# Optimization experiments

Hardware: AMD Instinct MI355X
Metric: run time of the kernel (lower is better)

Reference implementation:

```python
import jax, jax.numpy as jnp
import numpy as np
import math

B, S, D, H, FF = 2, 2048, 1024, 16, 4096
HD = D // H
EPS = 1e-5


def setup_inputs() -> dict:
    key = jax.random.key(0)
    ks = jax.random.split(key, 16)
    w = lambda k, shape: (jax.random.normal(k, shape, jnp.float32) * 0.02)
    future = jnp.triu(jnp.ones((S, S), dtype=bool), k=1)
    causal_mask = jnp.where(future, -jnp.inf, 0.0).astype(jnp.float32)
    return {
        "src": jax.random.normal(ks[0], (B, S, D), jnp.float32),
        "causal_mask": causal_mask,
        "Wq": w(ks[1], (D, D)), "bq": jnp.zeros((D,), jnp.float32),
        "Wk": w(ks[2], (D, D)), "bk": jnp.zeros((D,), jnp.float32),
        "Wv": w(ks[3], (D, D)), "bv": jnp.zeros((D,), jnp.float32),
        "Wo": w(ks[4], (D, D)), "bo": jnp.zeros((D,), jnp.float32),
        "W1": w(ks[5], (D, FF)), "b1": jnp.zeros((FF,), jnp.float32),
        "W2": w(ks[6], (FF, D)), "b2": jnp.zeros((D,), jnp.float32),
        "ln1_g": jnp.ones((D,), jnp.float32), "ln1_b": jnp.zeros((D,), jnp.float32),
        "ln2_g": jnp.ones((D,), jnp.float32), "ln2_b": jnp.zeros((D,), jnp.float32),
    }


def _layernorm(x, g, b):
    mu = jnp.mean(x, axis=-1, keepdims=True)
    var = jnp.mean((x - mu) ** 2, axis=-1, keepdims=True)
    return (x - mu) * jax.lax.rsqrt(var + EPS) * g + b


def reference(src, causal_mask, Wq, bq, Wk, bk, Wv, bv, Wo, bo,
              W1, b1, W2, b2, ln1_g, ln1_b, ln2_g, ln2_b):
    # QKV projections, split heads: [B,S,D] -> [B,H,S,HD]
    def split_heads(x):
        return x.reshape(B, S, H, HD).transpose(0, 2, 1, 3)

    q = split_heads(src @ Wq + bq)
    k = split_heads(src @ Wk + bk)
    v = split_heads(src @ Wv + bv)

    # scores: [B,H,S,S]; attn_mask = causal_mask broadcast over batch, then head dim
    scores = jnp.einsum("bhqd,bhkd->bhqk", q, k) / math.sqrt(HD)
    scores = scores + causal_mask[None, None, :, :]
    # scores[scores != scores] = 0
    scores = jnp.where(jnp.isnan(scores), 0.0, scores)
    # rows that are entirely inf -> 0
    mask_all_inf = jnp.all(jnp.isinf(scores), axis=-1, keepdims=True)
    scores = jnp.where(mask_all_inf, 0.0, scores)
    attn = jax.nn.softmax(scores, axis=-1)
    attn = jnp.where(jnp.isnan(attn), 0.0, attn)

    ctx = jnp.einsum("bhqk,bhkd->bhqd", attn, v)
    ctx = ctx.transpose(0, 2, 1, 3).reshape(B, S, D)
    attn_out = ctx @ Wo + bo

    x = _layernorm(src + attn_out, ln1_g, ln1_b)
    ff = jax.nn.relu(x @ W1 + b1) @ W2 + b2
    return _layernorm(x + ff, ln2_g, ln2_b)
```

## Files before the change

kernel.cpp:

```cpp
#include <hip/hip_runtime.h>

#define SS 2048
#define DD 1024
#define HH 16
#define HDIM 64
#define BB 2
#define FFD 4096
#define MR (BB*SS)
#define QKVLD 3072

typedef __bf16 bf16;
typedef __bf16 bf16x4 __attribute__((ext_vector_type(4)));
typedef __bf16 bf16x8 __attribute__((ext_vector_type(8)));
typedef float f32x4 __attribute__((ext_vector_type(4)));

struct P4 { bf16* p[4]; };

__device__ inline f32x4 mfma32(bf16x8 a, bf16x8 b, f32x4 c) {
  return __builtin_amdgcn_mfma_f32_16x16x32_bf16(a, b, c, 0, 0, 0);
}

__device__ inline void gload_lds16(const void* g, void* l) {
  __builtin_amdgcn_global_load_lds(
      (const __attribute__((address_space(1))) void*)g,
      (__attribute__((address_space(3))) void*)l, 16, 0, 0);
}

__global__ __launch_bounds__(256)
void cvt_bf16_kernel(const float* __restrict__ in, bf16* __restrict__ out, int n) {
  int i = (blockIdx.x * 256 + threadIdx.x) * 4;
  if (i >= n) return;
  float4 v = *(const float4*)(in + i);
  bf16x4 o;
  o[0] = (bf16)v.x; o[1] = (bf16)v.y; o[2] = (bf16)v.z; o[3] = (bf16)v.w;
  *(bf16x4*)(out + i) = o;
}

__global__ __launch_bounds__(256)
void concat_bias_kernel(const float* __restrict__ bq, const float* __restrict__ bk,
                        const float* __restrict__ bv, float* __restrict__ out) {
  int i = blockIdx.x * 256 + threadIdx.x;
  out[i] = i < 1024 ? bq[i] : (i < 2048 ? bk[i - 1024] : bv[i - 2048]);
}

__global__ __launch_bounds__(256)
void transpose_w_kernel(const float* __restrict__ W, bf16* __restrict__ Wt,
                        int K, int N) {
  __shared__ float t[32][33];
  int tx = threadIdx.x & 31, ty = threadIdx.x >> 5;
  int n0 = blockIdx.x * 32, k0 = blockIdx.y * 32;
  #pragma unroll
  for (int i = 0; i < 4; ++i)
    t[ty + i*8][tx] = W[(size_t)(k0 + ty + i*8) * N + n0 + tx];
  __syncthreads();
  #pragma unroll
  for (int i = 0; i < 4; ++i)
    Wt[(size_t)(n0 + ty + i*8) * K + k0 + tx] = (bf16)t[tx][ty + i*8];
}

__global__ __launch_bounds__(256)
void transpose_v_kernel(const bf16* __restrict__ V2d, bf16* __restrict__ Vt) {
  __shared__ bf16 t[32][33];
  int tx = threadIdx.x & 31, ty = threadIdx.x >> 5;
  int s0 = blockIdx.x * 32, d0 = blockIdx.y * 32;
  int bh = blockIdx.z;
  int b = bh >> 4, h = bh & 15;
  #pragma unroll
  for (int i = 0; i < 4; ++i)
    t[ty + i*8][tx] = V2d[(size_t)(b*SS + s0 + ty + i*8) * QKVLD + h*HDIM + d0 + tx];
  __syncthreads();
  #pragma unroll
  for (int i = 0; i < 4; ++i)
    Vt[((size_t)bh*HDIM + d0 + ty + i*8) * SS + s0 + tx] = t[tx][ty + i*8];
}

template<int OUT_BF16, int RELU, int SPLITK>
__global__ __launch_bounds__(512)
void gemm256(const bf16* __restrict__ A, const bf16* __restrict__ Bt,
             const float* __restrict__ bias, void* __restrict__ Cout,
             P4 part, int Ndim, int Kdim) {
  __shared__ bf16 Asm[2][256 * 64];
  __shared__ bf16 Bsm[2][256 * 64];
  const int gx = gridDim.x, gy = gridDim.y;
  const int gxy = gx * gy;
  const int nwg = gxy * gridDim.z;
  const int lin = (blockIdx.z * gy + blockIdx.y) * gx + blockIdx.x;
  const int swz = (lin & 7) * (nwg >> 3) + (lin >> 3);
  int bz = 0, rem = swz;
  if (SPLITK > 1) { bz = swz / gxy; rem = swz - bz * gxy; }
  const int by = rem / gx, bx = rem - by * gx;
  const int m0 = by * 256, n0 = bx * 256;
  const int tid = threadIdx.x;
  const int wave = tid >> 6, lane = tid & 63;
  const int g = lane >> 4, r = lane & 15;
  const int wr = wave >> 2, wn = wave & 3;
  const int kstart = bz * (Kdim / SPLITK);

  const int srow = wave * 8 + (lane >> 3);
  const int skslot = (lane & 7) ^ (lane >> 3);
  const bf16* Ag = A + (size_t)(m0 + srow) * Kdim + kstart + skslot * 8;
  const bf16* Bg = Bt + (size_t)(n0 + srow) * Kdim + kstart + skslot * 8;

  f32x4 acc[8][4] = {};
  const int NT = (Kdim / SPLITK) >> 6;

  auto stage = [&](int t) {
    const int kb = t << 6;
    bf16* Ad = Asm[t & 1];
    bf16* Bd = Bsm[t & 1];
    #pragma unroll
    for (int j = 0; j < 4; ++j)
      gload_lds16(Ag + (size_t)j * 64 * Kdim + kb, Ad + (j * 64 + wave * 8) * 64);
    #pragma unroll
    for (int j = 0; j < 4; ++j)
      gload_lds16(Bg + (size_t)j * 64 * Kdim + kb, Bd + (j * 64 + wave * 8) * 64);
  };

  stage(0);
  asm volatile("s_waitcnt vmcnt(0)" ::: "memory");
  asm volatile("s_barrier" ::: "memory");

  for (int t = 0; t < NT; ++t) {
    const bf16* Ab = Asm[t & 1];
    const bf16* Bb = Bsm[t & 1];
    #pragma unroll
    for (int ph = 0; ph < 4; ++ph) {
      const int mq = ph >> 1, nq = ph & 1;
      bf16x8 af[4][2], bfr[2][2];
      #pragma unroll
      for (int i = 0; i < 4; ++i) {
        const int row = wr * 128 + (mq * 4 + i) * 16 + r;
        #pragma unroll
        for (int kk = 0; kk < 2; ++kk)
          af[i][kk] = *(const bf16x8*)(Ab + row * 64 + (((kk * 4 + g) ^ (r & 7)) * 8));
      }
      #pragma unroll
      for (int i = 0; i < 2; ++i) {
        const int rowb = wn * 64 + (nq * 2 + i) * 16 + r;
        #pragma unroll
        for (int kk = 0; kk < 2; ++kk)
          bfr[i][kk] = *(const bf16x8*)(Bb + rowb * 64 + (((kk * 4 + g) ^ (r & 7)) * 8));
      }
      if (ph == 0 && t + 1 < NT) stage(t + 1);
      asm volatile("s_barrier" ::: "memory");
      __builtin_amdgcn_s_setprio(1);
      #pragma unroll
      for (int i = 0; i < 4; ++i)
        #pragma unroll
        for (int jn = 0; jn < 2; ++jn)
          #pragma unroll
          for (int kk = 0; kk < 2; ++kk)
            acc[mq * 4 + i][nq * 2 + jn] =
                mfma32(af[i][kk], bfr[jn][kk], acc[mq * 4 + i][nq * 2 + jn]);
      __builtin_amdgcn_s_setprio(0);
      asm volatile("s_barrier" ::: "memory");
    }
    asm volatile("s_waitcnt vmcnt(0)" ::: "memory");
    asm volatile("s_barrier" ::: "memory");
  }

  #pragma unroll
  for (int mi = 0; mi < 8; ++mi) {
    #pragma unroll
    for (int ni = 0; ni < 4; ++ni) {
      const int col = n0 + wn * 64 + ni * 16 + r;
      const float bv = (SPLITK > 1) ? 0.f : bias[col];
      #pragma unroll
      for (int jj = 0; jj < 4; ++jj) {
        const int row = m0 + wr * 128 + mi * 16 + g * 4 + jj;
        float v = acc[mi][ni][jj] + bv;
        if (RELU) v = fmaxf(v, 0.f);
        if (SPLITK > 1) part.p[bz][(size_t)row * Ndim + col] = (bf16)v;
        else if (OUT_BF16) ((bf16*)Cout)[(size_t)row * Ndim + col] = (bf16)v;
        else               ((float*)Cout)[(size_t)row * Ndim + col] = v;
      }
    }
  }
}

template<int OUT_BF16, int RELU, int SPLITK>
__global__ __launch_bounds__(256)
void gemm_bt(const bf16* __restrict__ A, const bf16* __restrict__ Bt,
             const float* __restrict__ bias, void* __restrict__ Cout,
             float* __restrict__ Cout2, int Mdim, int Ndim, int Kdim) {
  __shared__ bf16 As[128 * 32];
  __shared__ bf16 Bs[128 * 32];
  const int gx = gridDim.x, gy = gridDim.y;
  const int nwg = gx * gy * gridDim.z;
  const int lin = (blockIdx.z * gy + blockIdx.y) * gx + blockIdx.x;
  const int swz = (lin & 7) * (nwg >> 3) + (lin >> 3);
  const int bz = swz / (gx * gy);
  const int rem = swz - bz * gx * gy;
  const int by = rem / gx;
  const int bx = rem - by * gx;
  const int tid = threadIdx.x;
  const int wave = tid >> 6;
  const int lane = tid & 63;
  const int g = lane >> 4;
  const int r = lane & 15;
  const int m0 = by * 128;
  const int n0 = bx * 128;
  const int kchunk = Kdim / SPLITK;
  const int kstart = bz * kchunk;
  const int wr = wave >> 1, wc = wave & 1;
  f32x4 acc[4][4] = {};
  const int strow = tid >> 2;
  const int stcol = (tid & 3) * 8;
  const bf16* Abase = A + (size_t)(m0 + strow) * Kdim + kstart + stcol;
  const bf16* Bbase = Bt + (size_t)(n0 + strow) * Kdim + kstart + stcol;
  bf16* AsW = As + wave * 512;
  bf16* BsW = Bs + wave * 512;
  for (int k0 = 0; k0 < kchunk; k0 += 32) {
    __syncthreads();
    gload_lds16(Abase + k0, AsW);
    gload_lds16(Abase + k0 + (size_t)64 * Kdim, AsW + 2048);
    gload_lds16(Bbase + k0, BsW);
    gload_lds16(Bbase + k0 + (size_t)64 * Kdim, BsW + 2048);
    __syncthreads();
    bf16x8 af[4], bfr[4];
    #pragma unroll
    for (int i = 0; i < 4; ++i)
      af[i] = *(const bf16x8*)(As + (wr*64 + i*16 + r) * 32 + g * 8);
    #pragma unroll
    for (int i = 0; i < 4; ++i)
      bfr[i] = *(const bf16x8*)(Bs + (wc*64 + i*16 + r) * 32 + g * 8);
    #pragma unroll
    for (int mi = 0; mi < 4; ++mi)
      #pragma unroll
      for (int ni = 0; ni < 4; ++ni)
        acc[mi][ni] = mfma32(af[mi], bfr[ni], acc[mi][ni]);
  }
  float* outp = (SPLITK > 1 && bz) ? Cout2 : (float*)Cout;
  #pragma unroll
  for (int mi = 0; mi < 4; ++mi) {
    #pragma unroll
    for (int ni = 0; ni < 4; ++ni) {
      const int col = n0 + wc*64 + ni*16 + r;
      const float bv = (SPLITK > 1) ? 0.f : bias[col];
      #pragma unroll
      for (int j = 0; j < 4; ++j) {
        const int row = m0 + wr*64 + mi*16 + g*4 + j;
        float v = acc[mi][ni][j] + bv;
        if (RELU) v = fmaxf(v, 0.f);
        if (OUT_BF16) ((bf16*)Cout)[(size_t)row * Ndim + col] = (bf16)v;
        else          outp[(size_t)row * Ndim + col] = v;
      }
    }
  }
}

__global__ __launch_bounds__(256)
void attn_kernel(const bf16* __restrict__ Q2d, const bf16* __restrict__ K2d,
                 const bf16* __restrict__ Vt, bf16* __restrict__ ctx) {
  __shared__ bf16 Ks[2 * 4096];
  __shared__ bf16 Vs[2 * 4096];
  const int tid = threadIdx.x;
  const int wave = tid >> 6;
  const int lane = tid & 63;
  const int g = lane >> 4, r = lane & 15;
  const int lin = blockIdx.y * gridDim.x + blockIdx.x;
  const int swz = (lin & 7) * 64 + (lin >> 3);
  const int p = swz & 15;
  const int bh = swz >> 4;
  const int b = bh >> 4, h = bh & 15;

  const int strow = wave * 16 + (lane >> 2);
  const int lslot = (lane & 3) ^ ((lane >> 3) & 3);
  const bf16* srcK0 = K2d + (size_t)(b*SS + strow) * QKVLD + h*HDIM + lslot * 8;
  const bf16* srcK1 = srcK0 + 32;
  const bf16* srcV0 = Vt + ((size_t)bh*HDIM + strow) * SS + lslot * 8;
  const bf16* srcV1 = srcV0 + 32;

  auto sw = [](int row, int s) { return row * 32 + ((s ^ ((row >> 1) & 3)) * 8); };

  const int kr0 = 8 * (r >> 2) + (r & 3);
  const int oKa0 = sw(kr0,      g), oKb0 = 2048 + oKa0;
  const int oKa1 = sw(kr0 +  4, g), oKb1 = 2048 + oKa1;
  const int oKa2 = sw(kr0 + 32, g), oKb2 = 2048 + oKa2;
  const int oKa3 = sw(kr0 + 36, g), oKb3 = 2048 + oKa3;
  int oV[4];
  #pragma unroll
  for (int c = 0; c < 4; ++c) oV[c] = sw(c * 16 + r, g);

  #pragma unroll
  for (int tt = 0; tt < 2; ++tt) {
    const int tile = tt ? (31 - p) : p;
    const int q0 = tile * 64 + wave * 16;
    const int qg = q0 + r;
    const bf16* qp = Q2d + (size_t)(b*SS + q0 + r) * QKVLD + h * HDIM;
    const bf16x8 qf0 = *(const bf16x8*)(qp + g * 8);
    const bf16x8 qf1 = *(const bf16x8*)(qp + 32 + g * 8);
    f32x4 ov[4] = {};
    float m = -3.0e38f, l = 0.f;
    const int nst = tile + 1;
    {
      bf16* kb = Ks + wave * 512;
      bf16* vb = Vs + wave * 512;
      gload_lds16(srcK0, kb);
      gload_lds16(srcK1, kb + 2048);
      gload_lds16(srcV0, vb);
      gload_lds16(srcV1, vb + 2048);
    }
    __syncthreads();
    int cur = 0;
    for (int st = 0; st < nst; ++st) {
      const int k0 = st * 64;
      if (st + 1 < nst) {
        const int kn = k0 + 64;
        bf16* kb = Ks + (cur ^ 1) * 4096 + wave * 512;
        bf16* vb = Vs + (cur ^ 1) * 4096 + wave * 512;
        gload_lds16(srcK0 + (size_t)kn * QKVLD, kb);
        gload_lds16(srcK1 + (size_t)kn * QKVLD, kb + 2048);
        gload_lds16(srcV0 + kn, vb);
        gload_lds16(srcV1 + kn, vb + 2048);
      }
      const bf16* Kb = Ks + cur * 4096;
      const bf16* Vb = Vs + cur * 4096;
      f32x4 c0 = {}, c1 = {}, c2 = {}, c3 = {};
      __builtin_amdgcn_s_setprio(1);
      c0 = mfma32(*(const bf16x8*)(Kb + oKa0), qf0, c0);
      c1 = mfma32(*(const bf16x8*)(Kb + oKa1), qf0, c1);
      c2 = mfma32(*(const bf16x8*)(Kb + oKa2), qf0, c2);
      c3 = mfma32(*(const bf16x8*)(Kb + oKa3), qf0, c3);
      c0 = mfma32(*(const bf16x8*)(Kb + oKb0), qf1, c0);
      c1 = mfma32(*(const bf16x8*)(Kb + oKb1), qf1, c1);
      c2 = mfma32(*(const bf16x8*)(Kb + oKb2), qf1, c2);
      c3 = mfma32(*(const bf16x8*)(Kb + oKb3), qf1, c3);
      __builtin_amdgcn_s_setprio(0);
      float p0[4], p1[4], p2[4], p3[4];
      float tmax = -3.0e38f;
      const bool need_mask = (k0 + 63 > qg);
      #pragma unroll
      for (int j = 0; j < 4; ++j) {
        float s0 = c0[j] * 0.125f;
        float s1 = c1[j] * 0.125f;
        float s2 = c2[j] * 0.125f;
        float s3 = c3[j] * 0.125f;
        if (need_mask) {
          if (k0 + 8*g + j > qg)          s0 = -3.0e38f;
          if (k0 + 8*g + 4 + j > qg)      s1 = -3.0e38f;
          if (k0 + 32 + 8*g + j > qg)     s2 = -3.0e38f;
          if (k0 + 32 + 8*g + 4 + j > qg) s3 = -3.0e38f;
        }
        p0[j] = s0; p1[j] = s1; p2[j] = s2; p3[j] = s3;
        tmax = fmaxf(tmax, fmaxf(fmaxf(s0, s1), fmaxf(s2, s3)));
      }
      tmax = fmaxf(tmax, __shfl_xor(tmax, 16));
      tmax = fmaxf(tmax, __shfl_xor(tmax, 32));
      const float mnew = fmaxf(m, tmax);
      const float sc = __expf(m - mnew);
      float tsum = 0.f;
      #pragma unroll
      for (int j = 0; j < 4; ++j) {
        p0[j] = __expf(p0[j] - mnew);
        p1[j] = __expf(p1[j] - mnew);
        p2[j] = __expf(p2[j] - mnew);
        p3[j] = __expf(p3[j] - mnew);
        tsum += (p0[j] + p1[j]) + (p2[j] + p3[j]);
      }
      tsum += __shfl_xor(tsum, 16);
      tsum += __shfl_xor(tsum, 32);
      l = l * sc + tsum;
      m = mnew;
      bf16x8 pfa, pfb;
      #pragma unroll
      for (int j = 0; j < 4; ++j) {
        pfa[j] = (bf16)p0[j]; pfa[4 + j] = (bf16)p1[j];
        pfb[j] = (bf16)p2[j]; pfb[4 + j] = (bf16)p3[j];
      }
      #pragma unroll
      for (int j = 0; j < 4; ++j) {
        const float scj = __shfl(sc, 4*g + j);
        #pragma unroll
        for (int c = 0; c < 4; ++c) ov[c][j] *= scj;
      }
      __builtin_amdgcn_s_setprio(1);
      #pragma unroll
      for (int c = 0; c < 4; ++c) {
        bf16x8 vfa = *(const bf16x8*)(Vb + oV[c]);
        bf16x8 vfb = *(const bf16x8*)(Vb + 2048 + oV[c]);
        ov[c] = mfma32(pfa, vfa, ov[c]);
        ov[c] = mfma32(pfb, vfb, ov[c]);
      }
      __builtin_amdgcn_s_setprio(0);
      __syncthreads();
      cur ^= 1;
    }
    #pragma unroll
    for (int j = 0; j < 4; ++j) {
      const float lj = __shfl(l, 4*g + j);
      const float inv = 1.f / lj;
      const int row = b*SS + q0 + 4*g + j;
      #pragma unroll
      for (int c = 0; c < 4; ++c)
        ctx[(size_t)row * DD + h*HDIM + c*16 + r] = (bf16)(ov[c][j] * inv);
    }
  }
}

template<int NP, int HASB, int WRITEB>
__global__ __launch_bounds__(256)
void ln_kernel(const float* __restrict__ a, const float* __restrict__ p0,
               const float* __restrict__ p1, const float* __restrict__ cb,
               const float* __restrict__ gam, const float* __restrict__ bet,
               float* __restrict__ outf, bf16* __restrict__ outb) {
  const int row = blockIdx.x;
  const int tid = threadIdx.x;
  const size_t base = (size_t)row * DD + tid * 4;
  float4 va = *(const float4*)(a + base);
  float4 vc = *(const float4*)(p0 + base);
  float x0 = va.x + vc.x, x1 = va.y + vc.y, x2 = va.z + vc.z, x3 = va.w + vc.w;
  if (NP > 1) {
    float4 vp = *(const float4*)(p1 + base);
    x0 += vp.x; x1 += vp.y; x2 += vp.z; x3 += vp.w;
  }
  if (HASB) {
    float4 vb4 = *(const float4*)(cb + tid * 4);
    x0 += vb4.x; x1 += vb4.y; x2 += vb4.z; x3 += vb4.w;
  }
  float s  = x0 + x1 + x2 + x3;
  float s2 = x0*x0 + x1*x1 + x2*x2 + x3*x3;
  #pragma unroll
  for (int off = 32; off > 0; off >>= 1) {
    s  += __shfl_xor(s,  off);
    s2 += __shfl_xor(s2, off);
  }
  __shared__ float red[8];
  const int wv = tid >> 6;
  if ((tid & 63) == 0) { red[wv] = s; red[wv + 4] = s2; }
  __syncthreads();
  s  = red[0] + red[1] + red[2] + red[3];
  s2 = red[4] + red[5] + red[6] + red[7];
  const float mu  = s * (1.f / DD);
  const float var = s2 * (1.f / DD) - mu * mu;
  const float rs  = rsqrtf(var + 1e-5f);
  float4 vg = *(const float4*)(gam + tid * 4);
  float4 vb = *(const float4*)(bet + tid * 4);
  float y0 = (x0 - mu) * rs * vg.x + vb.x;
  float y1 = (x1 - mu) * rs * vg.y + vb.y;
  float y2 = (x2 - mu) * rs * vg.z + vb.z;
  float y3 = (x3 - mu) * rs * vg.w + vb.w;
  float4 yo; yo.x = y0; yo.y = y1; yo.z = y2; yo.w = y3;
  *(float4*)(outf + base) = yo;
  if (WRITEB) {
    bf16x4 ob;
    ob[0] = (bf16)y0; ob[1] = (bf16)y1; ob[2] = (bf16)y2; ob[3] = (bf16)y3;
    *(bf16x4*)(outb + base) = ob;
  }
}

__global__ __launch_bounds__(256)
void ln_bf4_kernel(const float* __restrict__ a, P4 part, const float* __restrict__ cb,
                   const float* __restrict__ gam, const float* __restrict__ bet,
                   float* __restrict__ outf) {
  const int row = blockIdx.x;
  const int tid = threadIdx.x;
  const size_t base = (size_t)row * DD + tid * 4;
  float4 va = *(const float4*)(a + base);
  bf16x4 u0 = *(const bf16x4*)(part.p[0] + base);
  bf16x4 u1 = *(const bf16x4*)(part.p[1] + base);
  bf16x4 u2 = *(const bf16x4*)(part.p[2] + base);
  bf16x4 u3 = *(const bf16x4*)(part.p[3] + base);
  float4 vb4 = *(const float4*)(cb + tid * 4);
  float x0 = va.x + ((float)u0[0] + (float)u1[0]) + ((float)u2[0] + (float)u3[0]) + vb4.x;
  float x1 = va.y + ((float)u0[1] + (float)u1[1]) + ((float)u2[1] + (float)u3[1]) + vb4.y;
  float x2 = va.z + ((float)u0[2] + (float)u1[2]) + ((float)u2[2] + (float)u3[2]) + vb4.z;
  float x3 = va.w + ((float)u0[3] + (float)u1[3]) + ((float)u2[3] + (float)u3[3]) + vb4.w;
  float s  = x0 + x1 + x2 + x3;
  float s2 = x0*x0 + x1*x1 + x2*x2 + x3*x3;
  #pragma unroll
  for (int off = 32; off > 0; off >>= 1) {
    s  += __shfl_xor(s,  off);
    s2 += __shfl_xor(s2, off);
  }
  __shared__ float red[8];
  const int wv = tid >> 6;
  if ((tid & 63) == 0) { red[wv] = s; red[wv + 4] = s2; }
  __syncthreads();
  s  = red[0] + red[1] + red[2] + red[3];
  s2 = red[4] + red[5] + red[6] + red[7];
  const float mu  = s * (1.f / DD);
  const float var = s2 * (1.f / DD) - mu * mu;
  const float rs  = rsqrtf(var + 1e-5f);
  float4 vg = *(const float4*)(gam + tid * 4);
  float4 vb = *(const float4*)(bet + tid * 4);
  float4 yo;
  yo.x = (x0 - mu) * rs * vg.x + vb.x;
  yo.y = (x1 - mu) * rs * vg.y + vb.y;
  yo.z = (x2 - mu) * rs * vg.z + vb.z;
  yo.w = (x3 - mu) * rs * vg.w + vb.w;
  *(float4*)(outf + base) = yo;
}

extern "C" void kernel_launch(void* const* d_in, const int* in_sizes, int n_in,
                              void* d_out, int out_size, void* d_ws, size_t ws_size,
                              hipStream_t stream) {
  const float* src  = (const float*)d_in[0];
  const float* Wq   = (const float*)d_in[2];
  const float* bq   = (const float*)d_in[3];
  const float* Wk   = (const float*)d_in[4];
  const float* bk   = (const float*)d_in[5];
  const float* Wv   = (const float*)d_in[6];
  const float* bv   = (const float*)d_in[7];
  const float* Wo   = (const float*)d_in[8];
  const float* bo   = (const float*)d_in[9];
  const float* W1   = (const float*)d_in[10];
  const float* b1   = (const float*)d_in[11];
  const float* W2   = (const float*)d_in[12];
  const float* b2   = (const float*)d_in[13];
  const float* ln1g = (const float*)d_in[14];
  const float* ln1b = (const float*)d_in[15];
  const float* ln2g = (const float*)d_in[16];
  const float* ln2b = (const float*)d_in[17];

  char* ws = (char*)d_ws;
  const size_t MB = 1024 * 1024;
  bf16* wqkvt = (bf16*)(ws + 0 * MB);
  bf16* wot   = (bf16*)(ws + 6 * MB);
  bf16* w1t   = (bf16*)(ws + 8 * MB);
  bf16* w2t   = (bf16*)(ws + 16 * MB);
  bf16* bsrc  = (bf16*)(ws + 24 * MB);
  bf16* xb    = bsrc;
  bf16* qkv   = (bf16*)(ws + 32 * MB);
  bf16* vt    = (bf16*)(ws + 56 * MB);
  bf16* ctx   = (bf16*)(ws + 64 * MB);
  bf16* ff1   = qkv;
  float* xf   = (float*)(ws + 72 * MB);
  float* bqkv = (float*)(ws + 88 * MB);
  float* wo_p1 = (float*)(ws + 32 * MB);
  float* attn_out = (float*)d_out;
  float* outp  = (float*)d_out;
  P4 fp;
  fp.p[0] = (bf16*)(ws + 0 * MB);
  fp.p[1] = (bf16*)(ws + 8 * MB);
  fp.p[2] = (bf16*)(ws + 24 * MB);
  fp.p[3] = (bf16*)(ws + 64 * MB);

  cvt_bf16_kernel<<<(MR * DD) / 1024, 256, 0, stream>>>(src, bsrc, MR * DD);
  transpose_w_kernel<<<dim3(32, 32), 256, 0, stream>>>(Wq, wqkvt,             DD, DD);
  transpose_w_kernel<<<dim3(32, 32), 256, 0, stream>>>(Wk, wqkvt + 1024*1024, DD, DD);
  transpose_w_kernel<<<dim3(32, 32), 256, 0, stream>>>(Wv, wqkvt + 2048*1024, DD, DD);
  transpose_w_kernel<<<dim3(32, 32), 256, 0, stream>>>(Wo, wot, DD, DD);
  transpose_w_kernel<<<dim3(128, 32), 256, 0, stream>>>(W1, w1t, DD, FFD);
  transpose_w_kernel<<<dim3(32, 128), 256, 0, stream>>>(W2, w2t, FFD, DD);
  concat_bias_kernel<<<12, 256, 0, stream>>>(bq, bk, bv, bqkv);

  gemm256<1, 0, 1><<<dim3(QKVLD / 256, MR / 256), 512, 0, stream>>>(bsrc, wqkvt, bqkv, qkv, P4{}, QKVLD, DD);
  transpose_v_kernel<<<dim3(SS / 32, HDIM / 32, BB * HH), 256, 0, stream>>>(qkv + 2048, vt);

  attn_kernel<<<dim3(16, BB * HH), 256, 0, stream>>>(qkv, qkv + 1024, vt, ctx);

  gemm_bt<0, 0, 2><<<dim3(8, 32, 2), 256, 0, stream>>>(ctx, wot, nullptr, attn_out, wo_p1, MR, DD, DD);
  ln_kernel<2, 1, 1><<<MR, 256, 0, stream>>>(src, attn_out, wo_p1, bo, ln1g, ln1b, xf, xb);

  gemm256<1, 1, 1><<<dim3(FFD / 256, MR / 256), 512, 0, stream>>>(xb, w1t, b1, ff1, P4{}, FFD, DD);
  gemm256<0, 0, 4><<<dim3(DD / 256, MR / 256, 4), 512, 0, stream>>>(ff1, w2t, nullptr, nullptr, fp, DD, FFD);
  ln_bf4_kernel<<<MR, 256, 0, stream>>>(xf, fp, b2, ln2g, ln2b, outp);
}
```

Baseline: 255.0 us.

## Split attention into one block per query tile with lazy exp2 softmax rescale

The attention kernel previously had each block process a paired light and heavy causal tile. Now each block handles a single 64-row query tile, so the grid doubles, and the heaviest tiles are scheduled first. The softmax works in the exp2 domain with the scale folded into one FMA, and it rescales the running max and accumulators only when a wave-level threshold is exceeded. The LDS swizzle also gains an extra XOR term to reduce bank conflicts. The trade-offs are more blocks, each reloading Q and K/V setup, and a bounded-overflow approach that depends on the threshold choice.

```diff
diff --git a/kernel.cpp b/kernel.cpp
--- a/kernel.cpp
+++ b/kernel.cpp
@@ -259,19 +259,21 @@
   const int lane = tid & 63;
   const int g = lane >> 4, r = lane & 15;
   const int lin = blockIdx.y * gridDim.x + blockIdx.x;
-  const int swz = (lin & 7) * 64 + (lin >> 3);
-  const int p = swz & 15;
-  const int bh = swz >> 4;
+  const int swz = (lin & 7) * 128 + (lin >> 3);
+  const int bh = swz >> 5;
+  const int tile = 31 - (swz & 31);
   const int b = bh >> 4, h = bh & 15;
 
   const int strow = wave * 16 + (lane >> 2);
-  const int lslot = (lane & 3) ^ ((lane >> 3) & 3);
+  const int lslot = (lane & 3) ^ ((lane >> 3) & 3) ^ ((2 * wave + (lane >> 5)) & 3);
   const bf16* srcK0 = K2d + (size_t)(b*SS + strow) * QKVLD + h*HDIM + lslot * 8;
   const bf16* srcK1 = srcK0 + 32;
   const bf16* srcV0 = Vt + ((size_t)bh*HDIM + strow) * SS + lslot * 8;
   const bf16* srcV1 = srcV0 + 32;
 
-  auto sw = [](int row, int s) { return row * 32 + ((s ^ ((row >> 1) & 3)) * 8); };
+  auto sw = [](int row, int s) {
+    return row * 32 + ((s ^ ((row >> 1) & 3) ^ ((row >> 3) & 3)) * 8);
+  };
 
   const int kr0 = 8 * (r >> 2) + (r & 3);
   const int oKa0 = sw(kr0,      g), oKb0 = 2048 + oKa0;
@@ -282,119 +284,124 @@
   #pragma unroll
   for (int c = 0; c < 4; ++c) oV[c] = sw(c * 16 + r, g);
 
-  #pragma unroll
-  for (int tt = 0; tt < 2; ++tt) {
-    const int tile = tt ? (31 - p) : p;
-    const int q0 = tile * 64 + wave * 16;
-    const int qg = q0 + r;
-    const bf16* qp = Q2d + (size_t)(b*SS + q0 + r) * QKVLD + h * HDIM;
-    const bf16x8 qf0 = *(const bf16x8*)(qp + g * 8);
-    const bf16x8 qf1 = *(const bf16x8*)(qp + 32 + g * 8);
-    f32x4 ov[4] = {};
-    float m = -3.0e38f, l = 0.f;
-    const int nst = tile + 1;
-    {
-      bf16* kb = Ks + wave * 512;
-      bf16* vb = Vs + wave * 512;
-      gload_lds16(srcK0, kb);
-      gload_lds16(srcK1, kb + 2048);
-      gload_lds16(srcV0, vb);
-      gload_lds16(srcV1, vb + 2048);
-    }
-    __syncthreads();
-    int cur = 0;
-    for (int st = 0; st < nst; ++st) {
-      const int k0 = st * 64;
-      if (st + 1 < nst) {
-        const int kn = k0 + 64;
-        bf16* kb = Ks + (cur ^ 1) * 4096 + wave * 512;
-        bf16* vb = Vs + (cur ^ 1) * 4096 + wave * 512;
-        gload_lds16(srcK0 + (size_t)kn * QKVLD, kb);
-        gload_lds16(srcK1 + (size_t)kn * QKVLD, kb + 2048);
-        gload_lds16(srcV0 + kn, vb);
-        gload_lds16(srcV1 + kn, vb + 2048);
+  const int q0 = tile * 64 + wave * 16;
+  const int qg = q0 + r;
+  const bf16* qp = Q2d + (size_t)(b*SS + q0 + r) * QKVLD + h * HDIM;
+  const bf16x8 qf0 = *(const bf16x8*)(qp + g * 8);
+  const bf16x8 qf1 = *(const bf16x8*)(qp + 32 + g * 8);
+  f32x4 ov[4] = {};
+  const float K2 = 0.18033688f;
+  float m2 = 0.f, l = 0.f;
+  const int nst = tile + 1;
+  {
+    bf16* kb = Ks + wave * 512;
+    bf16* vb = Vs + wave * 512;
+    gload_lds16(srcK0, kb);
+    gload_lds16(srcK1, kb + 2048);
+    gload_lds16(srcV0, vb);
+    gload_lds16(srcV1, vb + 2048);
+  }
+  __syncthreads();
+  int cur = 0;
+  for (int st = 0; st < nst; ++st) {
+    const int k0 = st * 64;
+    if (st + 1 < nst) {
+      const int kn = k0 + 64;
+      bf16* kb = Ks + (cur ^ 1) * 4096 + wave * 512;
+      bf16* vb = Vs + (cur ^ 1) * 4096 + wave * 512;
+      gload_lds16(srcK0 + (size_t)kn * QKVLD, kb);
+      gload_lds16(srcK1 + (size_t)kn * QKVLD, kb + 2048);
+      gload_lds16(srcV0 + kn, vb);
+      gload_lds16(srcV1 + kn, vb + 2048);
+    }
+    const bf16* Kb = Ks + cur * 4096;
+    const bf16* Vb = Vs + cur * 4096;
+    f32x4 c0 = {}, c1 = {}, c2 = {}, c3 = {};
+    __builtin_amdgcn_s_setprio(1);
+    c0 = mfma32(*(const bf16x8*)(Kb + oKa0), qf0, c0);
+    c1 = mfma32(*(const bf16x8*)(Kb + oKa1), qf0, c1);
+    c2 = mfma32(*(const bf16x8*)(Kb + oKa2), qf0, c2);
+    c3 = mfma32(*(const bf16x8*)(Kb + oKa3), qf0, c3);
+    c0 = mfma32(*(const bf16x8*)(Kb + oKb0), qf1, c0);
+    c1 = mfma32(*(const bf16x8*)(Kb + oKb1), qf1, c1);
+    c2 = mfma32(*(const bf16x8*)(Kb + oKb2), qf1, c2);
+    c3 = mfma32(*(const bf16x8*)(Kb + oKb3), qf1, c3);
+    __builtin_amdgcn_s_setprio(0);
+    float f0[4], f1[4], f2[4], f3[4];
+    float tmax = -3.0e38f;
+    #pragma unroll
+    for (int j = 0; j < 4; ++j) {
+      f0[j] = fmaf(c0[j], K2, -m2);
+      f1[j] = fmaf(c1[j], K2, -m2);
+      f2[j] = fmaf(c2[j], K2, -m2);
+      f3[j] = fmaf(c3[j], K2, -m2);
+    }
+    if (k0 + 63 > q0) {
+      #pragma unroll
+      for (int j = 0; j < 4; ++j) {
+        if (k0 + 8*g + j > qg)          f0[j] = -3.0e38f;
+        if (k0 + 8*g + 4 + j > qg)      f1[j] = -3.0e38f;
+        if (k0 + 32 + 8*g + j > qg)     f2[j] = -3.0e38f;
+        if (k0 + 32 + 8*g + 4 + j > qg) f3[j] = -3.0e38f;
       }
-      const bf16* Kb = Ks + cur * 4096;
-      const bf16* Vb = Vs + cur * 4096;
-      f32x4 c0 = {}, c1 = {}, c2 = {}, c3 = {};
-      __builtin_amdgcn_s_setprio(1);
-      c0 = mfma32(*(const bf16x8*)(Kb + oKa0), qf0, c0);
-      c1 = mfma32(*(const bf16x8*)(Kb + oKa1), qf0, c1);
-      c2 = mfma32(*(const bf16x8*)(Kb + oKa2), qf0, c2);
-      c3 = mfma32(*(const bf16x8*)(Kb + oKa3), qf0, c3);
-      c0 = mfma32(*(const bf16x8*)(Kb + oKb0), qf1, c0);
-      c1 = mfma32(*(const bf16x8*)(Kb + oKb1), qf1, c1);
-      c2 = mfma32(*(const bf16x8*)(Kb + oKb2), qf1, c2);
-      c3 = mfma32(*(const bf16x8*)(Kb + oKb3), qf1, c3);
-      __builtin_amdgcn_s_setprio(0);
-      float p0[4], p1[4], p2[4], p3[4];
-      float tmax = -3.0e38f;
-      const bool need_mask = (k0 + 63 > qg);
+    }
+    #pragma unroll
+    for (int j = 0; j < 4; ++j)
+      tmax = fmaxf(tmax, fmaxf(fmaxf(f0[j], f1[j]), fmaxf(f2[j], f3[j])));
+    tmax = fmaxf(tmax, __shfl_xor(tmax, 16));
+    tmax = fmaxf(tmax, __shfl_xor(tmax, 32));
+    if (__any(tmax > 11.54f)) {
+      const float rmp = fmaxf(tmax, 0.f);
+      m2 += rmp;
+      const float sc = exp2f(-rmp);
+      l *= sc;
       #pragma unroll
       for (int j = 0; j < 4; ++j) {
-        float s0 = c0[j] * 0.125f;
-        float s1 = c1[j] * 0.125f;
-        float s2 = c2[j] * 0.125f;
-        float s3 = c3[j] * 0.125f;
-        if (need_mask) {
-          if (k0 + 8*g + j > qg)          s0 = -3.0e38f;
-          if (k0 + 8*g + 4 + j > qg)      s1 = -3.0e38f;
-          if (k0 + 32 + 8*g + j > qg)     s2 = -3.0e38f;
-          if (k0 + 32 + 8*g + 4 + j > qg) s3 = -3.0e38f;
-        }
-        p0[j] = s0; p1[j] = s1; p2[j] = s2; p3[j] = s3;
-        tmax = fmaxf(tmax, fmaxf(fmaxf(s0, s1), fmaxf(s2, s3)));
-      }
-      tmax = fmaxf(tmax, __shfl_xor(tmax, 16));
-      tmax = fmaxf(tmax, __shfl_xor(tmax, 32));
-      const float mnew = fmaxf(m, tmax);
-      const float sc = __expf(m - mnew);
-      float tsum = 0.f;
-      #pragma unroll
-      for (int j = 0; j < 4; ++j) {
-        p0[j] = __expf(p0[j] - mnew);
-        p1[j] = __expf(p1[j] - mnew);
-        p2[j] = __expf(p2[j] - mnew);
-        p3[j] = __expf(p3[j] - mnew);
-        tsum += (p0[j] + p1[j]) + (p2[j] + p3[j]);
-      }
-      tsum += __shfl_xor(tsum, 16);
-      tsum += __shfl_xor(tsum, 32);
-      l = l * sc + tsum;
-      m = mnew;
-      bf16x8 pfa, pfb;
-      #pragma unroll
-      for (int j = 0; j < 4; ++j) {
-        pfa[j] = (bf16)p0[j]; pfa[4 + j] = (bf16)p1[j];
-        pfb[j] = (bf16)p2[j]; pfb[4 + j] = (bf16)p3[j];
-      }
-      #pragma unroll
-      for (int j = 0; j < 4; ++j) {
+        f0[j] -= rmp; f1[j] -= rmp; f2[j] -= rmp; f3[j] -= rmp;
         const float scj = __shfl(sc, 4*g + j);
         #pragma unroll
         for (int c = 0; c < 4; ++c) ov[c][j] *= scj;
       }
-      __builtin_amdgcn_s_setprio(1);
-      #pragma unroll
-      for (int c = 0; c < 4; ++c) {
-        bf16x8 vfa = *(const bf16x8*)(Vb + oV[c]);
-        bf16x8 vfb = *(const bf16x8*)(Vb + 2048 + oV[c]);
-        ov[c] = mfma32(pfa, vfa, ov[c]);
-        ov[c] = mfma32(pfb, vfb, ov[c]);
-      }
-      __builtin_amdgcn_s_setprio(0);
-      __syncthreads();
-      cur ^= 1;
-    }
+    }
+    float tsum = 0.f;
+    float p0[4], p1[4], p2[4], p3[4];
     #pragma unroll
     for (int j = 0; j < 4; ++j) {
-      const float lj = __shfl(l, 4*g + j);
-      const float inv = 1.f / lj;
-      const int row = b*SS + q0 + 4*g + j;
-      #pragma unroll
-      for (int c = 0; c < 4; ++c)
-        ctx[(size_t)row * DD + h*HDIM + c*16 + r] = (bf16)(ov[c][j] * inv);
-    }
+      p0[j] = exp2f(f0[j]);
+      p1[j] = exp2f(f1[j]);
+      p2[j] = exp2f(f2[j]);
+      p3[j] = exp2f(f3[j]);
+      tsum += (p0[j] + p1[j]) + (p2[j] + p3[j]);
+    }
+    tsum += __shfl_xor(tsum, 16);
+    tsum += __shfl_xor(tsum, 32);
+    l += tsum;
+    bf16x8 pfa, pfb;
+    #pragma unroll
+    for (int j = 0; j < 4; ++j) {
+      pfa[j] = (bf16)p0[j]; pfa[4 + j] = (bf16)p1[j];
+      pfb[j] = (bf16)p2[j]; pfb[4 + j] = (bf16)p3[j];
+    }
+    __builtin_amdgcn_s_setprio(1);
+    #pragma unroll
+    for (int c = 0; c < 4; ++c) {
+      bf16x8 vfa = *(const bf16x8*)(Vb + oV[c]);
+      bf16x8 vfb = *(const bf16x8*)(Vb + 2048 + oV[c]);
+      ov[c] = mfma32(pfa, vfa, ov[c]);
+      ov[c] = mfma32(pfb, vfb, ov[c]);
+    }
+    __builtin_amdgcn_s_setprio(0);
+    __syncthreads();
+    cur ^= 1;
+  }
+  #pragma unroll
+  for (int j = 0; j < 4; ++j) {
+    const float lj = __shfl(l, 4*g + j);
+    const float inv = 1.f / lj;
+    const int row = b*SS + q0 + 4*g + j;
+    #pragma unroll
+    for (int c = 0; c < 4; ++c)
+      ctx[(size_t)row * DD + h*HDIM + c*16 + r] = (bf16)(ov[c][j] * inv);
   }
 }
 
@@ -548,7 +555,7 @@
   gemm256<1, 0, 1><<<dim3(QKVLD / 256, MR / 256), 512, 0, stream>>>(bsrc, wqkvt, bqkv, qkv, P4{}, QKVLD, DD);
   transpose_v_kernel<<<dim3(SS / 32, HDIM / 32, BB * HH), 256, 0, stream>>>(qkv + 2048, vt);
 
-  attn_kernel<<<dim3(16, BB * HH), 256, 0, stream>>>(qkv, qkv + 1024, vt, ctx);
+  attn_kernel<<<dim3(32, 32), 256, 0, stream>>>(qkv, qkv + 1024, vt, ctx);
 
   gemm_bt<0, 0, 2><<<dim3(8, 32, 2), 256, 0, stream>>>(ctx, wot, nullptr, attn_out, wo_p1, MR, DD, DD);
   ln_kernel<2, 1, 1><<<MR, 256, 0, stream>>>(src, attn_out, wo_p1, bo, ln1g, ln1b, xf, xb);
```

After: 283.7 us. 11.2% more time.
